# Kernel optimization log

Measured on AMD Instinct MI355X. Metric: run time of the kernel, lower is better.

Reference implementation:

```python
import jax, jax.numpy as jnp
import numpy as np


def setup_inputs() -> dict:
    key = jax.random.key(0)
    k1, k2 = jax.random.split(key)
    x = jax.random.normal(k1, (8, 8192, 512), dtype=jnp.float32)
    codebook = jax.random.normal(k2, (1024, 512), dtype=jnp.float32)
    return {"x": x, "codebook": codebook}


def reference(x, codebook):
    # torch.cdist -> Euclidean distance; argmin is invariant under sqrt, so
    x2 = jnp.sum(x * x, axis=-1, keepdims=True)          # [B, N, 1]
    c2 = jnp.sum(codebook * codebook, axis=-1)           # [K]
    xc = jnp.einsum('bnd,kd->bnk', x, codebook)          # [B, N, K]
    d2 = x2 - 2.0 * xc + c2                              # [B, N, K]
    idx = jnp.argmin(d2, axis=-1)                        # [B, N]
    return codebook[idx]                                 # [B, N, dim]
```

## Files before the change

kernel.cpp:

```cpp
#include <hip/hip_runtime.h>
#include <cstdio>


typedef float f32x4 __attribute__((ext_vector_type(4)));
typedef _Float16 half8 __attribute__((ext_vector_type(8)));

#define KDIM 512
#define NCODES 1024
#define NQ 65536
#define TAU_S 0.05f

#define WS_CBH   0ull
#define WS_C2H   1048576ull
#define WS_C2D   1052672ull
#define WS_CBT   1060864ull
#define WS_IDX   3158016ull
#define WS_LIST  3420160ull
#define WS_CTR   3682304ull
#define WS_NEED  (WS_CTR + 4ull)

__device__ __forceinline__ unsigned short f2h(float f) {
  _Float16 h = (_Float16)f;
  return __builtin_bit_cast(unsigned short, h);
}

__device__ __forceinline__ void async16(const void* g, void* l) {
  __builtin_amdgcn_global_load_lds(
      (const __attribute__((address_space(1))) void*)g,
      (__attribute__((address_space(3))) void*)l, 16, 0, 0);
}

__global__ __launch_bounds__(256) void vq_prep(const float* __restrict__ cb,
                                               unsigned short* __restrict__ cbh,
                                               float* __restrict__ c2h,
                                               double* __restrict__ c2d) {
  int lane = threadIdx.x & 63;
  int row = blockIdx.x * 4 + (threadIdx.x >> 6);
  const float4* src = (const float4*)(cb + (size_t)row * KDIM);
  float4 u = src[lane * 2], v = src[lane * 2 + 1];
  double p = (double)u.x * u.x + (double)u.y * u.y + (double)u.z * u.z + (double)u.w * u.w +
             (double)v.x * v.x + (double)v.y * v.y + (double)v.z * v.z + (double)v.w * v.w;
#pragma unroll
  for (int m = 1; m < 64; m <<= 1) p += __shfl_xor(p, m);
  if (lane == 0) { c2h[row] = (float)(0.5 * p); c2d[row] = 0.5 * p; }
  unsigned r0 = f2h(u.x) | ((unsigned)f2h(u.y) << 16);
  unsigned r1 = f2h(u.z) | ((unsigned)f2h(u.w) << 16);
  unsigned r2 = f2h(v.x) | ((unsigned)f2h(v.y) << 16);
  unsigned r3 = f2h(v.z) | ((unsigned)f2h(v.w) << 16);
  *(int4*)(cbh + (size_t)row * KDIM + lane * 8) = make_int4((int)r0, (int)r1, (int)r2, (int)r3);
}

__global__ __launch_bounds__(256, 1) void vq_main(const float* __restrict__ x,
                                                  const unsigned short* __restrict__ cbh,
                                                  const float* __restrict__ c2h,
                                                  int* __restrict__ idx,
                                                  int* __restrict__ list,
                                                  int* __restrict__ counter) {
  __shared__ __align__(16) char pool[135168];
  float* c2s = (float*)(pool + 131072);

  const int tid = threadIdx.x;
  const int lane = tid & 63, wv = tid >> 6;
  const int c = lane & 15, q = lane >> 4;
  const int qbase = blockIdx.x * 256 + wv * 64;

#define STAGE(cc) do {                                                        \
    const unsigned short* _s = cbh + (size_t)(cc) * 32768;                    \
    char* _d = pool + (((cc) & 1) * 65536);                                   \
    _Pragma("unroll")                                                         \
    for (int s = 0; s < 16; ++s) {                                            \
      int r = wv * 16 + s;                                                    \
      async16(_s + (size_t)r * 512 + ((lane ^ (r & 7)) * 8),                  \
              _d + r * 1024 + lane * 16);                                     \
    } } while (0)

  async16(c2h + wv * 256 + lane * 4, pool + 131072 + wv * 1024 + lane * 16);
  STAGE(0);

  half8 a[4][16];
#pragma unroll
  for (int rf = 0; rf < 4; ++rf) {
    const float* xr = x + (size_t)(qbase + rf * 16 + c) * KDIM + q * 8;
    float4 t[32];
#pragma unroll
    for (int kf = 0; kf < 16; ++kf) {
      t[kf * 2]     = *(const float4*)(xr + kf * 32);
      t[kf * 2 + 1] = *(const float4*)(xr + kf * 32 + 4);
    }
#pragma unroll
    for (int kf = 0; kf < 16; ++kf) {
      float4 lo = t[kf * 2], hi = t[kf * 2 + 1];
      half8 h;
      h[0] = (_Float16)lo.x; h[1] = (_Float16)lo.y;
      h[2] = (_Float16)lo.z; h[3] = (_Float16)lo.w;
      h[4] = (_Float16)hi.x; h[5] = (_Float16)hi.y;
      h[6] = (_Float16)hi.z; h[7] = (_Float16)hi.w;
      a[rf][kf] = h;
    }
    __builtin_amdgcn_sched_barrier(0);
  }

  float m1[4][4], m2[4][4];
  int mcx[4][4];
#pragma unroll
  for (int i = 0; i < 4; ++i)
#pragma unroll
    for (int r = 0; r < 4; ++r) { m1[i][r] = 1e30f; m2[i][r] = 1e30f; mcx[i][r] = 0; }

  const int m3 = c & 7;

#pragma unroll 1
  for (int ch = 0; ch < 16; ++ch) {
    __syncthreads();
    if (ch + 1 < 16) STAGE(ch + 1);

    const unsigned short* B = (const unsigned short*)(pool + ((ch & 1) * 65536));
    f32x4 acc[4][4];
#pragma unroll
    for (int i = 0; i < 4; ++i)
#pragma unroll
      for (int j = 0; j < 4; ++j) acc[i][j] = (f32x4){0.f, 0.f, 0.f, 0.f};

#pragma unroll
    for (int kf = 0; kf < 16; ++kf) {
      half8 b[4];
      const int gg = (kf * 4 + q) ^ m3;
#pragma unroll
      for (int cf = 0; cf < 4; ++cf)
        b[cf] = *(const half8*)&B[(cf * 16 + c) * 512 + gg * 8];
#pragma unroll
      for (int i = 0; i < 4; ++i)
#pragma unroll
        for (int cf = 0; cf < 4; ++cf)
          acc[i][cf] = __builtin_amdgcn_mfma_f32_16x16x32_f16(a[i][kf], b[cf], acc[i][cf], 0, 0, 0);
    }
#pragma unroll
    for (int cf = 0; cf < 4; ++cf) {
      const int col = ch * 64 + cf * 16 + c;
      const float c2v = c2s[col];
#pragma unroll
      for (int i = 0; i < 4; ++i)
#pragma unroll
        for (int r = 0; r < 4; ++r) {
          float sv = c2v - acc[i][cf][r];
          float hi = fmaxf(sv, m1[i][r]);
          m2[i][r] = fminf(m2[i][r], hi);
          bool lt = sv < m1[i][r];
          m1[i][r] = lt ? sv : m1[i][r];
          mcx[i][r] = lt ? col : mcx[i][r];
        }
    }
  }
#undef STAGE

#pragma unroll
  for (int m = 1; m < 16; m <<= 1) {
#pragma unroll
    for (int i = 0; i < 4; ++i)
#pragma unroll
      for (int r = 0; r < 4; ++r) {
        float o1 = __shfl_xor(m1[i][r], m);
        float o2 = __shfl_xor(m2[i][r], m);
        int   oc = __shfl_xor(mcx[i][r], m);
        float hi = fmaxf(o1, m1[i][r]);
        m2[i][r] = fminf(fminf(m2[i][r], o2), hi);
        bool lt = o1 < m1[i][r];
        m1[i][r] = lt ? o1 : m1[i][r];
        mcx[i][r] = lt ? oc : mcx[i][r];
      }
  }
  if (c == 0) {
#pragma unroll
    for (int i = 0; i < 4; ++i)
#pragma unroll
      for (int r = 0; r < 4; ++r) {
        int query = qbase + i * 16 + q * 4 + r;
        idx[query] = mcx[i][r];
        if (m2[i][r] - m1[i][r] < TAU_S) { int p = atomicAdd(counter, 1); list[p] = query; }
      }
  }
}

__global__ __launch_bounds__(256) void vq_trans(const float4* __restrict__ cb4,
                                                float4* __restrict__ cbT4) {
  __shared__ float t[64][65];
  const int bc = blockIdx.x >> 3, bk = blockIdx.x & 7;
  const int c0 = bc * 64, k0 = bk * 64;
  const int r = threadIdx.x >> 4, q4 = threadIdx.x & 15;
#pragma unroll
  for (int p = 0; p < 4; ++p) {
    int row = p * 16 + r;
    float4 v = cb4[(size_t)(c0 + row) * 128 + (k0 >> 2) + q4];
    t[row][q4 * 4 + 0] = v.x; t[row][q4 * 4 + 1] = v.y;
    t[row][q4 * 4 + 2] = v.z; t[row][q4 * 4 + 3] = v.w;
  }
  __syncthreads();
#pragma unroll
  for (int p = 0; p < 4; ++p) {
    int kk = p * 16 + r;
    float4 v = make_float4(t[q4 * 4 + 0][kk], t[q4 * 4 + 1][kk],
                           t[q4 * 4 + 2][kk], t[q4 * 4 + 3][kk]);
    cbT4[(size_t)(k0 + kk) * 256 + (c0 >> 2) + q4] = v;
  }
}

__global__ __launch_bounds__(256) void vq_refine(const float* __restrict__ x,
                                                 const float4* __restrict__ cbT4,
                                                 const double* __restrict__ c2d,
                                                 const int* __restrict__ list,
                                                 const int* __restrict__ counter,
                                                 int* __restrict__ idx) {
  __shared__ float xs[512];
  __shared__ double rv[4];
  __shared__ int rc[4];
  const int cnt = counter[0];
  const int tid = threadIdx.x, lane = tid & 63, wv = tid >> 6;
  for (int qi = blockIdx.x; qi < cnt; qi += gridDim.x) {
    const int query = list[qi];
    __syncthreads();
    xs[tid] = x[(size_t)query * KDIM + tid];
    xs[tid + 256] = x[(size_t)query * KDIM + tid + 256];
    __syncthreads();
    double a0 = 0, a1 = 0, a2 = 0, a3 = 0;
    const float4* xs4 = (const float4*)xs;
#pragma unroll 4
    for (int k4 = 0; k4 < 128; ++k4) {
      float4 xv = xs4[k4];
      float4 c0 = cbT4[(k4 * 4 + 0) * 256 + tid];
      float4 c1 = cbT4[(k4 * 4 + 1) * 256 + tid];
      float4 c2v = cbT4[(k4 * 4 + 2) * 256 + tid];
      float4 c3 = cbT4[(k4 * 4 + 3) * 256 + tid];
      a0 = fma((double)xv.x, (double)c0.x, a0);
      a1 = fma((double)xv.x, (double)c0.y, a1);
      a2 = fma((double)xv.x, (double)c0.z, a2);
      a3 = fma((double)xv.x, (double)c0.w, a3);
      a0 = fma((double)xv.y, (double)c1.x, a0);
      a1 = fma((double)xv.y, (double)c1.y, a1);
      a2 = fma((double)xv.y, (double)c1.z, a2);
      a3 = fma((double)xv.y, (double)c1.w, a3);
      a0 = fma((double)xv.z, (double)c2v.x, a0);
      a1 = fma((double)xv.z, (double)c2v.y, a1);
      a2 = fma((double)xv.z, (double)c2v.z, a2);
      a3 = fma((double)xv.z, (double)c2v.w, a3);
      a0 = fma((double)xv.w, (double)c3.x, a0);
      a1 = fma((double)xv.w, (double)c3.y, a1);
      a2 = fma((double)xv.w, (double)c3.z, a2);
      a3 = fma((double)xv.w, (double)c3.w, a3);
    }
    double best = c2d[tid * 4] - a0;
    int bc = tid * 4;
    double s1 = c2d[tid * 4 + 1] - a1;
    if (s1 < best) { best = s1; bc = tid * 4 + 1; }
    double s2 = c2d[tid * 4 + 2] - a2;
    if (s2 < best) { best = s2; bc = tid * 4 + 2; }
    double s3 = c2d[tid * 4 + 3] - a3;
    if (s3 < best) { best = s3; bc = tid * 4 + 3; }
#pragma unroll
    for (int m = 1; m < 64; m <<= 1) {
      double o = __shfl_xor(best, m);
      int oc = __shfl_xor(bc, m);
      if (o < best) { best = o; bc = oc; }
    }
    if (lane == 0) { rv[wv] = best; rc[wv] = bc; }
    __syncthreads();
    if (tid == 0) {
      double b = rv[0]; int bci = rc[0];
#pragma unroll
      for (int w = 1; w < 4; ++w)
        if (rv[w] < b) { b = rv[w]; bci = rc[w]; }
      idx[query] = bci;
    }
    __syncthreads();
  }
}

__global__ __launch_bounds__(256) void vq_gather(const float* __restrict__ cb,
                                                 const int* __restrict__ idx,
                                                 float* __restrict__ out) {
  size_t i = (size_t)blockIdx.x * 256 + threadIdx.x;
  int qg = (int)(i >> 7), d = (int)(i & 127);
  ((float4*)out)[i] = ((const float4*)cb)[(size_t)idx[qg] * 128 + d];
}

extern "C" void kernel_launch(void* const* d_in, const int* in_sizes, int n_in,
                              void* d_out, int out_size, void* d_ws, size_t ws_size,
                              hipStream_t stream) {
  const float* x = (const float*)d_in[0];
  const float* cb = (const float*)d_in[1];
  float* out = (float*)d_out;
  char* ws = (char*)d_ws;
  if (ws_size < WS_NEED) {
    fprintf(stderr, "vq: ws_size %zu too small (need %llu)\n", ws_size,
            (unsigned long long)WS_NEED);
    return;
  }
  unsigned short* cbh = (unsigned short*)(ws + WS_CBH);
  float* c2h = (float*)(ws + WS_C2H);
  double* c2d = (double*)(ws + WS_C2D);
  float* cbT = (float*)(ws + WS_CBT);
  int* idx = (int*)(ws + WS_IDX);
  int* list = (int*)(ws + WS_LIST);
  int* counter = (int*)(ws + WS_CTR);

  hipMemsetAsync(counter, 0, 4, stream);
  vq_prep<<<256, 256, 0, stream>>>(cb, cbh, c2h, c2d);
  vq_trans<<<128, 256, 0, stream>>>((const float4*)cb, (float4*)cbT);
  vq_main<<<256, 256, 0, stream>>>(x, cbh, c2h, idx, list, counter);
  vq_refine<<<2048, 256, 0, stream>>>(x, (const float4*)cbT, c2d, list, counter, idx);
  vq_gather<<<32768, 256, 0, stream>>>(cb, idx, out);
}
```

Measured before the change: 401.6 us.

## Triple-buffer codebook staging with 8-wave blocks; fuse transpose into prep; stride gather

New measurement: 353.7 us. 1.14x faster.

```diff
diff --git a/kernel.cpp b/kernel.cpp
--- a/kernel.cpp
+++ b/kernel.cpp
@@ -30,133 +30,175 @@
       (__attribute__((address_space(3))) void*)l, 16, 0, 0);
 }
 
+#define SB0 __builtin_amdgcn_sched_barrier(0)
+
 __global__ __launch_bounds__(256) void vq_prep(const float* __restrict__ cb,
                                                unsigned short* __restrict__ cbh,
                                                float* __restrict__ c2h,
-                                               double* __restrict__ c2d) {
-  int lane = threadIdx.x & 63;
-  int row = blockIdx.x * 4 + (threadIdx.x >> 6);
-  const float4* src = (const float4*)(cb + (size_t)row * KDIM);
-  float4 u = src[lane * 2], v = src[lane * 2 + 1];
-  double p = (double)u.x * u.x + (double)u.y * u.y + (double)u.z * u.z + (double)u.w * u.w +
-             (double)v.x * v.x + (double)v.y * v.y + (double)v.z * v.z + (double)v.w * v.w;
-#pragma unroll
-  for (int m = 1; m < 64; m <<= 1) p += __shfl_xor(p, m);
-  if (lane == 0) { c2h[row] = (float)(0.5 * p); c2d[row] = 0.5 * p; }
-  unsigned r0 = f2h(u.x) | ((unsigned)f2h(u.y) << 16);
-  unsigned r1 = f2h(u.z) | ((unsigned)f2h(u.w) << 16);
-  unsigned r2 = f2h(v.x) | ((unsigned)f2h(v.y) << 16);
-  unsigned r3 = f2h(v.z) | ((unsigned)f2h(v.w) << 16);
-  *(int4*)(cbh + (size_t)row * KDIM + lane * 8) = make_int4((int)r0, (int)r1, (int)r2, (int)r3);
-}
-
-__global__ __launch_bounds__(256, 1) void vq_main(const float* __restrict__ x,
+                                               double* __restrict__ c2d,
+                                               float4* __restrict__ cbT4) {
+  __shared__ float t[64][65];
+  if (blockIdx.x < 256) {
+    int lane = threadIdx.x & 63;
+    int row = blockIdx.x * 4 + (threadIdx.x >> 6);
+    const float4* src = (const float4*)(cb + (size_t)row * KDIM);
+    float4 u = src[lane * 2], v = src[lane * 2 + 1];
+    double p = (double)u.x * u.x + (double)u.y * u.y + (double)u.z * u.z + (double)u.w * u.w +
+               (double)v.x * v.x + (double)v.y * v.y + (double)v.z * v.z + (double)v.w * v.w;
+#pragma unroll
+    for (int m = 1; m < 64; m <<= 1) p += __shfl_xor(p, m);
+    if (lane == 0) { c2h[row] = (float)(0.5 * p); c2d[row] = 0.5 * p; }
+    unsigned r0 = f2h(u.x) | ((unsigned)f2h(u.y) << 16);
+    unsigned r1 = f2h(u.z) | ((unsigned)f2h(u.w) << 16);
+    unsigned r2 = f2h(v.x) | ((unsigned)f2h(v.y) << 16);
+    unsigned r3 = f2h(v.z) | ((unsigned)f2h(v.w) << 16);
+    *(int4*)(cbh + (size_t)row * KDIM + lane * 8) = make_int4((int)r0, (int)r1, (int)r2, (int)r3);
+    return;
+  }
+  const int bb = blockIdx.x - 256;
+  const float4* cb4 = (const float4*)cb;
+  const int bc = bb >> 3, bk = bb & 7;
+  const int c0 = bc * 64, k0 = bk * 64;
+  const int r = threadIdx.x >> 4, q4 = threadIdx.x & 15;
+#pragma unroll
+  for (int p = 0; p < 4; ++p) {
+    int row = p * 16 + r;
+    float4 v = cb4[(size_t)(c0 + row) * 128 + (k0 >> 2) + q4];
+    t[row][q4 * 4 + 0] = v.x; t[row][q4 * 4 + 1] = v.y;
+    t[row][q4 * 4 + 2] = v.z; t[row][q4 * 4 + 3] = v.w;
+  }
+  __syncthreads();
+#pragma unroll
+  for (int p = 0; p < 4; ++p) {
+    int kk = p * 16 + r;
+    float4 v = make_float4(t[q4 * 4 + 0][kk], t[q4 * 4 + 1][kk],
+                           t[q4 * 4 + 2][kk], t[q4 * 4 + 3][kk]);
+    cbT4[(size_t)(k0 + kk) * 256 + (c0 >> 2) + q4] = v;
+  }
+}
+
+__global__ __launch_bounds__(512, 2) void vq_main(const float* __restrict__ x,
                                                   const unsigned short* __restrict__ cbh,
                                                   const float* __restrict__ c2h,
                                                   int* __restrict__ idx,
                                                   int* __restrict__ list,
                                                   int* __restrict__ counter) {
-  __shared__ __align__(16) char pool[135168];
-  float* c2s = (float*)(pool + 131072);
+  __shared__ __align__(16) char pool[102400];
+  float* c2s = (float*)(pool + 98304);
 
   const int tid = threadIdx.x;
   const int lane = tid & 63, wv = tid >> 6;
   const int c = lane & 15, q = lane >> 4;
-  const int qbase = blockIdx.x * 256 + wv * 64;
-
-#define STAGE(cc) do {                                                        \
-    const unsigned short* _s = cbh + (size_t)(cc) * 32768;                    \
-    char* _d = pool + (((cc) & 1) * 65536);                                   \
+  const int qbase = blockIdx.x * 256 + wv * 32;
+  const int Sc = ((c & 1) << 2) | ((c >> 1) & 3);
+
+#define STAGE(ch2, sb) do {                                                   \
+    const unsigned short* _s = cbh + (size_t)(ch2) * 16384;                   \
+    char* _d = pool + (sb) * 32768;                                           \
     _Pragma("unroll")                                                         \
-    for (int s = 0; s < 16; ++s) {                                            \
-      int r = wv * 16 + s;                                                    \
-      async16(_s + (size_t)r * 512 + ((lane ^ (r & 7)) * 8),                  \
-              _d + r * 1024 + lane * 16);                                     \
+    for (int s = 0; s < 4; ++s) {                                             \
+      int r = wv * 4 + s;                                                     \
+      int Sr = ((r & 1) << 2) | ((r >> 1) & 3);                               \
+      async16(_s + r * 512 + ((lane ^ Sr) * 8), _d + r * 1024 + lane * 16);   \
     } } while (0)
 
-  async16(c2h + wv * 256 + lane * 4, pool + 131072 + wv * 1024 + lane * 16);
-  STAGE(0);
-
-  half8 a[4][16];
-#pragma unroll
-  for (int rf = 0; rf < 4; ++rf) {
+  if (wv < 4) async16(c2h + wv * 256 + lane * 4, pool + 98304 + wv * 1024 + lane * 16);
+  STAGE(0, 0);
+  STAGE(1, 1);
+  SB0;
+
+  half8 a[2][16];
+#pragma unroll
+  for (int rf = 0; rf < 2; ++rf) {
     const float* xr = x + (size_t)(qbase + rf * 16 + c) * KDIM + q * 8;
-    float4 t[32];
-#pragma unroll
-    for (int kf = 0; kf < 16; ++kf) {
-      t[kf * 2]     = *(const float4*)(xr + kf * 32);
-      t[kf * 2 + 1] = *(const float4*)(xr + kf * 32 + 4);
-    }
-#pragma unroll
-    for (int kf = 0; kf < 16; ++kf) {
-      float4 lo = t[kf * 2], hi = t[kf * 2 + 1];
-      half8 h;
-      h[0] = (_Float16)lo.x; h[1] = (_Float16)lo.y;
-      h[2] = (_Float16)lo.z; h[3] = (_Float16)lo.w;
-      h[4] = (_Float16)hi.x; h[5] = (_Float16)hi.y;
-      h[6] = (_Float16)hi.z; h[7] = (_Float16)hi.w;
-      a[rf][kf] = h;
-    }
-    __builtin_amdgcn_sched_barrier(0);
-  }
-
-  float m1[4][4], m2[4][4];
-  int mcx[4][4];
-#pragma unroll
-  for (int i = 0; i < 4; ++i)
+#pragma unroll
+    for (int blk = 0; blk < 4; ++blk) {
+      float4 t[8];
+#pragma unroll
+      for (int s = 0; s < 4; ++s) {
+        int kf = blk * 4 + s;
+        t[s * 2]     = *(const float4*)(xr + kf * 32);
+        t[s * 2 + 1] = *(const float4*)(xr + kf * 32 + 4);
+      }
+#pragma unroll
+      for (int s = 0; s < 4; ++s) {
+        float4 lo = t[s * 2], hi = t[s * 2 + 1];
+        half8 h;
+        h[0] = (_Float16)lo.x; h[1] = (_Float16)lo.y;
+        h[2] = (_Float16)lo.z; h[3] = (_Float16)lo.w;
+        h[4] = (_Float16)hi.x; h[5] = (_Float16)hi.y;
+        h[6] = (_Float16)hi.z; h[7] = (_Float16)hi.w;
+        a[rf][blk * 4 + s] = h;
+      }
+    }
+  }
+  SB0;
+
+  float m1[2][4], m2[2][4];
+  int mcx[2][4];
+#pragma unroll
+  for (int i = 0; i < 2; ++i)
 #pragma unroll
     for (int r = 0; r < 4; ++r) { m1[i][r] = 1e30f; m2[i][r] = 1e30f; mcx[i][r] = 0; }
 
-  const int m3 = c & 7;
-
+#define BODY(cur, chv) do {                                                   \
+    const unsigned short* B = (const unsigned short*)(pool + (cur) * 32768);  \
+    f32x4 acc[2][2];                                                          \
+    acc[0][0] = (f32x4){0.f,0.f,0.f,0.f}; acc[0][1] = (f32x4){0.f,0.f,0.f,0.f};\
+    acc[1][0] = (f32x4){0.f,0.f,0.f,0.f}; acc[1][1] = (f32x4){0.f,0.f,0.f,0.f};\
+    _Pragma("unroll")                                                         \
+    for (int kf = 0; kf < 16; ++kf) {                                         \
+      const int gg = (kf * 4 + q) ^ Sc;                                       \
+      half8 b0 = *(const half8*)&B[(size_t)c * 512 + gg * 8];                 \
+      half8 b1 = *(const half8*)&B[(size_t)(16 + c) * 512 + gg * 8];          \
+      acc[0][0] = __builtin_amdgcn_mfma_f32_16x16x32_f16(a[0][kf], b0, acc[0][0], 0, 0, 0); \
+      acc[1][0] = __builtin_amdgcn_mfma_f32_16x16x32_f16(a[1][kf], b0, acc[1][0], 0, 0, 0); \
+      acc[0][1] = __builtin_amdgcn_mfma_f32_16x16x32_f16(a[0][kf], b1, acc[0][1], 0, 0, 0); \
+      acc[1][1] = __builtin_amdgcn_mfma_f32_16x16x32_f16(a[1][kf], b1, acc[1][1], 0, 0, 0); \
+    }                                                                         \
+    _Pragma("unroll")                                                         \
+    for (int cf = 0; cf < 2; ++cf) {                                          \
+      const int col = (chv) * 32 + cf * 16 + c;                               \
+      const float c2v = c2s[col];                                             \
+      _Pragma("unroll")                                                       \
+      for (int i = 0; i < 2; ++i)                                             \
+        _Pragma("unroll")                                                     \
+        for (int r = 0; r < 4; ++r) {                                         \
+          float sv = c2v - acc[i][cf][r];                                     \
+          float hi = fmaxf(sv, m1[i][r]);                                     \
+          m2[i][r] = fminf(m2[i][r], hi);                                     \
+          bool lt = sv < m1[i][r];                                            \
+          m1[i][r] = lt ? sv : m1[i][r];                                      \
+          mcx[i][r] = lt ? col : mcx[i][r];                                   \
+        }                                                                     \
+    } } while (0)
+
+  int cur = 0;
 #pragma unroll 1
-  for (int ch = 0; ch < 16; ++ch) {
-    __syncthreads();
-    if (ch + 1 < 16) STAGE(ch + 1);
-
-    const unsigned short* B = (const unsigned short*)(pool + ((ch & 1) * 65536));
-    f32x4 acc[4][4];
-#pragma unroll
-    for (int i = 0; i < 4; ++i)
-#pragma unroll
-      for (int j = 0; j < 4; ++j) acc[i][j] = (f32x4){0.f, 0.f, 0.f, 0.f};
-
-#pragma unroll
-    for (int kf = 0; kf < 16; ++kf) {
-      half8 b[4];
-      const int gg = (kf * 4 + q) ^ m3;
-#pragma unroll
-      for (int cf = 0; cf < 4; ++cf)
-        b[cf] = *(const half8*)&B[(cf * 16 + c) * 512 + gg * 8];
-#pragma unroll
-      for (int i = 0; i < 4; ++i)
-#pragma unroll
-        for (int cf = 0; cf < 4; ++cf)
-          acc[i][cf] = __builtin_amdgcn_mfma_f32_16x16x32_f16(a[i][kf], b[cf], acc[i][cf], 0, 0, 0);
-    }
-#pragma unroll
-    for (int cf = 0; cf < 4; ++cf) {
-      const int col = ch * 64 + cf * 16 + c;
-      const float c2v = c2s[col];
-#pragma unroll
-      for (int i = 0; i < 4; ++i)
-#pragma unroll
-        for (int r = 0; r < 4; ++r) {
-          float sv = c2v - acc[i][cf][r];
-          float hi = fmaxf(sv, m1[i][r]);
-          m2[i][r] = fminf(m2[i][r], hi);
-          bool lt = sv < m1[i][r];
-          m1[i][r] = lt ? sv : m1[i][r];
-          mcx[i][r] = lt ? col : mcx[i][r];
-        }
-    }
-  }
+  for (int ch = 0; ch < 31; ++ch) {
+    asm volatile("s_waitcnt vmcnt(4)" ::: "memory");
+    SB0;
+    __builtin_amdgcn_s_barrier();
+    SB0;
+    if (ch < 30) {
+      int sb = cur + 2; if (sb >= 3) sb -= 3;
+      STAGE(ch + 2, sb);
+    }
+    BODY(cur, ch);
+    cur = cur + 1; if (cur == 3) cur = 0;
+  }
+  asm volatile("s_waitcnt vmcnt(0)" ::: "memory");
+  SB0;
+  __builtin_amdgcn_s_barrier();
+  SB0;
+  BODY(cur, 31);
 #undef STAGE
+#undef BODY
 
 #pragma unroll
   for (int m = 1; m < 16; m <<= 1) {
 #pragma unroll
-    for (int i = 0; i < 4; ++i)
+    for (int i = 0; i < 2; ++i)
 #pragma unroll
       for (int r = 0; r < 4; ++r) {
         float o1 = __shfl_xor(m1[i][r], m);
@@ -171,36 +213,13 @@
   }
   if (c == 0) {
 #pragma unroll
-    for (int i = 0; i < 4; ++i)
+    for (int i = 0; i < 2; ++i)
 #pragma unroll
       for (int r = 0; r < 4; ++r) {
         int query = qbase + i * 16 + q * 4 + r;
         idx[query] = mcx[i][r];
         if (m2[i][r] - m1[i][r] < TAU_S) { int p = atomicAdd(counter, 1); list[p] = query; }
       }
-  }
-}
-
-__global__ __launch_bounds__(256) void vq_trans(const float4* __restrict__ cb4,
-                                                float4* __restrict__ cbT4) {
-  __shared__ float t[64][65];
-  const int bc = blockIdx.x >> 3, bk = blockIdx.x & 7;
-  const int c0 = bc * 64, k0 = bk * 64;
-  const int r = threadIdx.x >> 4, q4 = threadIdx.x & 15;
-#pragma unroll
-  for (int p = 0; p < 4; ++p) {
-    int row = p * 16 + r;
-    float4 v = cb4[(size_t)(c0 + row) * 128 + (k0 >> 2) + q4];
-    t[row][q4 * 4 + 0] = v.x; t[row][q4 * 4 + 1] = v.y;
-    t[row][q4 * 4 + 2] = v.z; t[row][q4 * 4 + 3] = v.w;
-  }
-  __syncthreads();
-#pragma unroll
-  for (int p = 0; p < 4; ++p) {
-    int kk = p * 16 + r;
-    float4 v = make_float4(t[q4 * 4 + 0][kk], t[q4 * 4 + 1][kk],
-                           t[q4 * 4 + 2][kk], t[q4 * 4 + 3][kk]);
-    cbT4[(size_t)(k0 + kk) * 256 + (c0 >> 2) + q4] = v;
   }
 }
 
@@ -277,9 +296,16 @@
 __global__ __launch_bounds__(256) void vq_gather(const float* __restrict__ cb,
                                                  const int* __restrict__ idx,
                                                  float* __restrict__ out) {
+  const size_t total = (size_t)NQ * 128;
+  const size_t stride = (size_t)2048 * 256;
   size_t i = (size_t)blockIdx.x * 256 + threadIdx.x;
-  int qg = (int)(i >> 7), d = (int)(i & 127);
-  ((float4*)out)[i] = ((const float4*)cb)[(size_t)idx[qg] * 128 + d];
+#pragma unroll 1
+  for (; i < total; i += stride) {
+    int qg = (int)(i >> 7), d = (int)(i & 127);
+    const f32x4* src = (const f32x4*)(cb + (size_t)idx[qg] * KDIM + d * 4);
+    f32x4 v = *src;
+    __builtin_nontemporal_store(v, (f32x4*)(out + i * 4));
+  }
 }
 
 extern "C" void kernel_launch(void* const* d_in, const int* in_sizes, int n_in,
@@ -303,9 +329,8 @@
   int* counter = (int*)(ws + WS_CTR);
 
   hipMemsetAsync(counter, 0, 4, stream);
-  vq_prep<<<256, 256, 0, stream>>>(cb, cbh, c2h, c2d);
-  vq_trans<<<128, 256, 0, stream>>>((const float4*)cb, (float4*)cbT);
-  vq_main<<<256, 256, 0, stream>>>(x, cbh, c2h, idx, list, counter);
+  vq_prep<<<384, 256, 0, stream>>>(cb, cbh, c2h, c2d, (float4*)cbT);
+  vq_main<<<256, 512, 0, stream>>>(x, cbh, c2h, idx, list, counter);
   vq_refine<<<2048, 256, 0, stream>>>(x, (const float4*)cbT, c2d, list, counter, idx);
-  vq_gather<<<32768, 256, 0, stream>>>(cb, idx, out);
-}
+  vq_gather<<<2048, 256, 0, stream>>>(cb, idx, out);
+}
```
